# Kernel tuning notes

Hardware: AMD Instinct MI355X
Metric: run time of the kernel (lower is better)

Reference implementation:

```python
import jax, jax.numpy as jnp
import numpy as np

N_EMBD = 1024
HEADS = 16
HEAD_DIM = N_EMBD // HEADS


def setup_inputs() -> dict:
    key = jax.random.key(0)
    k1, k2 = jax.random.split(key)
    x = jax.random.normal(k1, (2, 2048, N_EMBD), dtype=jnp.float32)
    W_qkv = jax.random.normal(k2, (N_EMBD, 3 * N_EMBD), dtype=jnp.float32) * (N_EMBD ** -0.5)
    b_qkv = jnp.zeros((3 * N_EMBD,), dtype=jnp.float32)
    return {"x": x, "W_qkv": W_qkv, "b_qkv": b_qkv}


def reference(x, W_qkv, b_qkv):
    B, T, _ = x.shape
    qkv = x @ W_qkv + b_qkv                      # [B, T, 3*n_embd]
    q, k, v = jnp.split(qkv, 3, axis=-1)
    q = q.reshape(B, T, HEADS, HEAD_DIM)
    k = k.reshape(B, T, HEADS, HEAD_DIM)
    v = v.reshape(B, T, HEADS, HEAD_DIM)
    attn = jnp.einsum('bthd,bThd->bhtT', q, k) / jnp.sqrt(jnp.float32(HEAD_DIM))
    causal = jnp.tril(jnp.ones((T, T), dtype=bool))  # [T, T]
    attn = jnp.where(causal, attn, -jnp.inf)
    attn = jax.nn.softmax(attn, axis=-1)
    # dropout is identity in deterministic/eval mode (training=False)
    out = jnp.einsum('bhtT,bThd->bthd', attn, v).reshape(B, T, N_EMBD)
    return out
```

## Files before the change

### kernel.cpp

```cpp
#include <hip/hip_runtime.h>
#include <hip/hip_bf16.h>

#define BATCH 2
#define TSEQ  2048
#define NEMBD 1024
#define HEADS 16
#define HDIM  64

typedef short          bf16x8 __attribute__((ext_vector_type(8)));
typedef float          f32x4  __attribute__((ext_vector_type(4)));
typedef unsigned short u16;

__device__ __forceinline__ u16 f2bf(float f) {
  unsigned int u = __float_as_uint(f);
  u += 0x7fffu + ((u >> 16) & 1u);
  return (u16)(u >> 16);
}

__device__ __forceinline__ void gld16(const u16* g, u16* l) {
  __builtin_amdgcn_global_load_lds(
      (const __attribute__((address_space(1))) unsigned int*)g,
      (__attribute__((address_space(3))) unsigned int*)l, 16, 0, 0);
}

__global__ __launch_bounds__(256) void k_convert_x(const float* __restrict__ x,
                                                   u16* __restrict__ xb) {
  int i = blockIdx.x * 256 + threadIdx.x;
  float4 v = ((const float4*)x)[i];
  ushort4 o;
  o.x = f2bf(v.x); o.y = f2bf(v.y); o.z = f2bf(v.z); o.w = f2bf(v.w);
  ((ushort4*)xb)[i] = o;
}

__global__ __launch_bounds__(256) void k_transpose_w(const float* __restrict__ w,
                                                     u16* __restrict__ wt) {
  __shared__ float tile[32][33];
  const int n0 = blockIdx.x * 32;
  const int k0 = blockIdx.y * 32;
  const int t  = threadIdx.x;
  const int r  = t >> 3;
  const int c4 = (t & 7) * 4;
  float4 v = *(const float4*)(w + (size_t)(k0 + r) * 3072 + n0 + c4);
  tile[r][c4 + 0] = v.x; tile[r][c4 + 1] = v.y;
  tile[r][c4 + 2] = v.z; tile[r][c4 + 3] = v.w;
  __syncthreads();
  ushort4 o;
  o.x = f2bf(tile[c4 + 0][r]);
  o.y = f2bf(tile[c4 + 1][r]);
  o.z = f2bf(tile[c4 + 2][r]);
  o.w = f2bf(tile[c4 + 3][r]);
  *(ushort4*)(wt + (size_t)(n0 + r) * 1024 + k0 + c4) = o;
}

__global__ __launch_bounds__(256, 3) void k_qkv_gemm(
    const u16* __restrict__ xb, const u16* __restrict__ wt,
    const float* __restrict__ bias,
    u16* __restrict__ qb, u16* __restrict__ kbuf, u16* __restrict__ vt) {
  __shared__ __align__(16) u16 As[128 * 64];
  __shared__ __align__(16) u16 Bs[128 * 64];

  const int t    = threadIdx.x;
  const int wv   = t >> 6;
  const int lane = t & 63;
  const int m    = lane & 15;
  const int quad = lane >> 4;
  const int lin  = blockIdx.x;
  const int cp   = lin >> 5;
  const int rp   = ((lin & 7) << 2) | ((lin >> 3) & 3);
  const int row0 = rp * 128;
  const int col0 = cp * 128;
  const int wr   = (wv >> 1) * 64;
  const int wc   = (wv & 1) * 64;

  const int sr = wv * 32 + (lane >> 3);
  const int gs = (lane & 7) ^ (sr & 7);
  const u16* ag = xb + (size_t)(row0 + sr) * 1024 + gs * 8;
  const u16* bg = wt + (size_t)(col0 + sr) * 1024 + gs * 8;
  u16* al = As + (wv * 32) * 64;
  u16* bl = Bs + (wv * 32) * 64;

  f32x4 acc[4][4];
  const f32x4 zf = {0.f, 0.f, 0.f, 0.f};
  for (int i = 0; i < 4; ++i)
    for (int j = 0; j < 4; ++j) acc[i][j] = zf;

  for (int kt = 0; kt < 16; ++kt) {
    const int kk = kt * 64;
    __syncthreads();
    gld16(ag + kk,             al);
    gld16(ag + kk +  8 * 1024, al +  8 * 64);
    gld16(ag + kk + 16 * 1024, al + 16 * 64);
    gld16(ag + kk + 24 * 1024, al + 24 * 64);
    gld16(bg + kk,             bl);
    gld16(bg + kk +  8 * 1024, bl +  8 * 64);
    gld16(bg + kk + 16 * 1024, bl + 16 * 64);
    gld16(bg + kk + 24 * 1024, bl + 24 * 64);
    __syncthreads();

#pragma unroll
    for (int h = 0; h < 2; ++h) {
      const int g = ((quad + 4 * h) ^ (m & 7)) * 8;
      bf16x8 af[4], bfr[4];
#pragma unroll
      for (int mt = 0; mt < 4; ++mt)
        af[mt] = *(const bf16x8*)(As + (wr + mt * 16 + m) * 64 + g);
#pragma unroll
      for (int nt = 0; nt < 4; ++nt)
        bfr[nt] = *(const bf16x8*)(Bs + (wc + nt * 16 + m) * 64 + g);
#pragma unroll
      for (int mt = 0; mt < 4; ++mt)
#pragma unroll
        for (int nt = 0; nt < 4; ++nt)
          acc[mt][nt] = __builtin_amdgcn_mfma_f32_16x16x32_bf16(
              af[mt], bfr[nt], acc[mt][nt], 0, 0, 0);
    }
  }

  const int sec = col0 >> 10;
#pragma unroll
  for (int nt = 0; nt < 4; ++nt) {
    const int Cc = col0 + wc + nt * 16 + m;
    const float bv = bias[Cc];
    const int c = Cc & 1023;
    const int h = c >> 6;
    const int d = c & 63;
#pragma unroll
    for (int mt = 0; mt < 4; ++mt) {
      const int Rbase = row0 + wr + mt * 16 + quad * 4;
      const int bb = Rbase >> 11;
      const int t0 = Rbase & 2047;
      const int bh = bb * HEADS + h;
      if (sec == 0) {
#pragma unroll
        for (int rg = 0; rg < 4; ++rg) {
          float v = (acc[mt][nt][rg] + bv) * 0.125f;
          qb[(size_t)(bh * TSEQ + t0 + rg) * HDIM + d] = f2bf(v);
        }
      } else if (sec == 1) {
#pragma unroll
        for (int rg = 0; rg < 4; ++rg) {
          float v = acc[mt][nt][rg] + bv;
          kbuf[(size_t)(bh * TSEQ + t0 + rg) * HDIM + d] = f2bf(v);
        }
      } else {
        ushort4 pk;
        pk.x = f2bf(acc[mt][nt][0] + bv);
        pk.y = f2bf(acc[mt][nt][1] + bv);
        pk.z = f2bf(acc[mt][nt][2] + bv);
        pk.w = f2bf(acc[mt][nt][3] + bv);
        *(ushort4*)(vt + (size_t)(bh * HDIM + d) * TSEQ + t0) = pk;
      }
    }
  }
}

__global__ __launch_bounds__(256, 3) void k_attn(
    const u16* __restrict__ qb, const u16* __restrict__ kbuf,
    const u16* __restrict__ vt, float* __restrict__ out) {
  __shared__ __align__(16) u16 Kb[2][4096];
  __shared__ __align__(16) u16 Vb[2][4096];
  __shared__ __align__(16) u16 pt[4][2 * 1152];

  const int t     = threadIdx.x;
  const int wv    = t >> 6;
  const int lane  = t & 63;
  const int m     = lane & 15;
  const int quad  = lane >> 4;
  const int bh    = blockIdx.x & 31;
  const int qtg   = 15 - (blockIdx.x >> 5);
  const int qbase = (qtg * 4 + wv) * 32;
  const int nkt   = 2 * qtg + 2;
  const int maskTile = qbase >> 6;

  u16* pw0 = &pt[wv][0];
  u16* pw1 = &pt[wv][1152];

  const u16* qrow0 = qb + ((size_t)bh * TSEQ + qbase + m) * HDIM + quad * 8;
  const u16* qrow1 = qrow0 + 16 * HDIM;
  bf16x8 aq0g0 = *(const bf16x8*)(qrow0);
  bf16x8 aq1g0 = *(const bf16x8*)(qrow0 + 32);
  bf16x8 aq0g1 = *(const bf16x8*)(qrow1);
  bf16x8 aq1g1 = *(const bf16x8*)(qrow1 + 32);

  const int sr = wv * 16 + (lane >> 3);
  const int gs = (lane & 7) ^ (sr & 7);
  const u16* kg = kbuf + ((size_t)bh * TSEQ + sr) * HDIM + gs * 8;
  const u16* vg = vt + ((size_t)bh * HDIM + sr) * TSEQ + gs * 8;
  u16* klds = &Kb[0][wv * 16 * 64];
  u16* vlds = &Vb[0][wv * 16 * 64];

  const int swL = (quad ^ (m & 7)) * 8;
  const int swH = ((quad + 4) ^ (m & 7)) * 8;

  f32x4 o0[4], o1[4];
  const f32x4 zf = {0.f, 0.f, 0.f, 0.f};
  for (int nt = 0; nt < 4; ++nt) { o0[nt] = zf; o1[nt] = zf; }
  float rsum0 = 0.f, rsum1 = 0.f;
  const int qi0 = qbase + m;
  const int qi1 = qbase + 16 + m;

  gld16(kg,             klds);
  gld16(kg + 8 * HDIM,  klds + 8 * 64);
  gld16(vg,             vlds);
  gld16(vg + 8 * TSEQ,  vlds + 8 * 64);
  __syncthreads();

  for (int kt = 0; kt < nkt; ++kt) {
    const int b = kt & 1;
    const u16* kb0 = &Kb[b][0];
    const u16* vb0 = &Vb[b][0];
    const bool active = (kt <= maskTile);

    bf16x8 vfL[4], vfH[4];
    f32x4 s0[4], s1[4];

    if (active) {
      for (int nt = 0; nt < 4; ++nt) { s0[nt] = zf; s1[nt] = zf; }
#pragma unroll
      for (int nt = 0; nt < 4; ++nt) {
        bf16x8 kf = *(const bf16x8*)(kb0 + (nt * 16 + m) * 64 + swL);
        s0[nt] = __builtin_amdgcn_mfma_f32_16x16x32_bf16(kf, aq0g0, s0[nt], 0, 0, 0);
        s1[nt] = __builtin_amdgcn_mfma_f32_16x16x32_bf16(kf, aq0g1, s1[nt], 0, 0, 0);
      }
#pragma unroll
      for (int nt = 0; nt < 4; ++nt) {
        bf16x8 kf = *(const bf16x8*)(kb0 + (nt * 16 + m) * 64 + swH);
        s0[nt] = __builtin_amdgcn_mfma_f32_16x16x32_bf16(kf, aq1g0, s0[nt], 0, 0, 0);
        s1[nt] = __builtin_amdgcn_mfma_f32_16x16x32_bf16(kf, aq1g1, s1[nt], 0, 0, 0);
      }

      if (kt == maskTile) {
        const int kb_ = kt * 64 + quad * 4;
#pragma unroll
        for (int nt = 0; nt < 4; ++nt)
#pragma unroll
          for (int rg = 0; rg < 4; ++rg) {
            const int kj = kb_ + nt * 16 + rg;
            if (kj > qi0) s0[nt][rg] = -1e30f;
            if (kj > qi1) s1[nt][rg] = -1e30f;
          }
      }

#pragma unroll
      for (int nt = 0; nt < 4; ++nt) {
        float p0 = __expf(s0[nt][0]), p1 = __expf(s0[nt][1]);
        float p2 = __expf(s0[nt][2]), p3 = __expf(s0[nt][3]);
        rsum0 += (p0 + p1) + (p2 + p3);
        ushort4 pk = {f2bf(p0), f2bf(p1), f2bf(p2), f2bf(p3)};
        *(ushort4*)(pw0 + m * 72 + nt * 16 + quad * 4) = pk;
      }

#pragma unroll
      for (int nt = 0; nt < 4; ++nt) {
        vfL[nt] = *(const bf16x8*)(vb0 + (nt * 16 + m) * 64 + swL);
        vfH[nt] = *(const bf16x8*)(vb0 + (nt * 16 + m) * 64 + swH);
      }
    }

    if (kt + 1 < nkt) {
      const int nb = (kt + 1) & 1;
      const u16* kgn = kg + (size_t)(kt + 1) * 64 * HDIM;
      const u16* vgn = vg + (kt + 1) * 64;
      u16* kl = &Kb[nb][wv * 16 * 64];
      u16* vl = &Vb[nb][wv * 16 * 64];
      gld16(kgn,            kl);
      gld16(kgn + 8 * HDIM, kl + 8 * 64);
      gld16(vgn,            vl);
      gld16(vgn + 8 * TSEQ, vl + 8 * 64);
    }

    if (active) {
      bf16x8 bp00 = *(const bf16x8*)(pw0 + m * 72 + quad * 8);
      bf16x8 bp01 = *(const bf16x8*)(pw0 + m * 72 + 32 + quad * 8);
#pragma unroll
      for (int nt = 0; nt < 4; ++nt)
        o0[nt] = __builtin_amdgcn_mfma_f32_16x16x32_bf16(vfL[nt], bp00, o0[nt], 0, 0, 0);
#pragma unroll
      for (int nt = 0; nt < 4; ++nt)
        o0[nt] = __builtin_amdgcn_mfma_f32_16x16x32_bf16(vfH[nt], bp01, o0[nt], 0, 0, 0);

#pragma unroll
      for (int nt = 0; nt < 4; ++nt) {
        float p0 = __expf(s1[nt][0]), p1 = __expf(s1[nt][1]);
        float p2 = __expf(s1[nt][2]), p3 = __expf(s1[nt][3]);
        rsum1 += (p0 + p1) + (p2 + p3);
        ushort4 pk = {f2bf(p0), f2bf(p1), f2bf(p2), f2bf(p3)};
        *(ushort4*)(pw1 + m * 72 + nt * 16 + quad * 4) = pk;
      }
      bf16x8 bp10 = *(const bf16x8*)(pw1 + m * 72 + quad * 8);
      bf16x8 bp11 = *(const bf16x8*)(pw1 + m * 72 + 32 + quad * 8);
#pragma unroll
      for (int nt = 0; nt < 4; ++nt)
        o1[nt] = __builtin_amdgcn_mfma_f32_16x16x32_bf16(vfL[nt], bp10, o1[nt], 0, 0, 0);
#pragma unroll
      for (int nt = 0; nt < 4; ++nt)
        o1[nt] = __builtin_amdgcn_mfma_f32_16x16x32_bf16(vfH[nt], bp11, o1[nt], 0, 0, 0);
    }

    __syncthreads();
  }

  rsum0 += __shfl_xor(rsum0, 16);
  rsum0 += __shfl_xor(rsum0, 32);
  rsum1 += __shfl_xor(rsum1, 16);
  rsum1 += __shfl_xor(rsum1, 32);
  const float inv0 = 1.0f / rsum0;
  const float inv1 = 1.0f / rsum1;

  const int bb = bh >> 4;
  const int h  = bh & 15;
  float* ob0 = out + ((size_t)(bb * TSEQ + qi0) * NEMBD + h * HDIM + quad * 4);
  float* ob1 = out + ((size_t)(bb * TSEQ + qi1) * NEMBD + h * HDIM + quad * 4);
#pragma unroll
  for (int nt = 0; nt < 4; ++nt) {
    float4 st;
    st.x = o0[nt][0] * inv0; st.y = o0[nt][1] * inv0;
    st.z = o0[nt][2] * inv0; st.w = o0[nt][3] * inv0;
    *(float4*)(ob0 + nt * 16) = st;
    float4 su;
    su.x = o1[nt][0] * inv1; su.y = o1[nt][1] * inv1;
    su.z = o1[nt][2] * inv1; su.w = o1[nt][3] * inv1;
    *(float4*)(ob1 + nt * 16) = su;
  }
}

extern "C" void kernel_launch(void* const* d_in, const int* in_sizes, int n_in,
                              void* d_out, int out_size, void* d_ws, size_t ws_size,
                              hipStream_t stream) {
  (void)in_sizes; (void)n_in; (void)out_size; (void)ws_size;
  const float* x    = (const float*)d_in[0];
  const float* W    = (const float*)d_in[1];
  const float* bqkv = (const float*)d_in[2];
  float* out = (float*)d_out;

  u16* ws   = (u16*)d_ws;
  u16* qb   = ws;
  u16* kbuf = ws + 4194304;
  u16* vt   = ws + 2 * 4194304;
  u16* xb   = ws + 3 * 4194304;
  u16* wt   = ws + 4 * 4194304;

  hipLaunchKernelGGL(k_convert_x, dim3(4096), dim3(256), 0, stream, x, xb);
  hipLaunchKernelGGL(k_transpose_w, dim3(96, 32), dim3(256), 0, stream, W, wt);
  hipLaunchKernelGGL(k_qkv_gemm, dim3(768), dim3(256), 0, stream,
                     xb, wt, bqkv, qb, kbuf, vt);
  hipLaunchKernelGGL(k_attn, dim3(512), dim3(256), 0, stream,
                     qb, kbuf, vt, out);
}
```

Baseline: 149.7 us.

## Merge prep kernels and retile attention into 64-query blocks with balanced scheduling

```diff
diff --git a/kernel.cpp b/kernel.cpp
--- a/kernel.cpp
+++ b/kernel.cpp
@@ -23,33 +23,36 @@
       (__attribute__((address_space(3))) unsigned int*)l, 16, 0, 0);
 }
 
-__global__ __launch_bounds__(256) void k_convert_x(const float* __restrict__ x,
-                                                   u16* __restrict__ xb) {
-  int i = blockIdx.x * 256 + threadIdx.x;
-  float4 v = ((const float4*)x)[i];
-  ushort4 o;
-  o.x = f2bf(v.x); o.y = f2bf(v.y); o.z = f2bf(v.z); o.w = f2bf(v.w);
-  ((ushort4*)xb)[i] = o;
-}
-
-__global__ __launch_bounds__(256) void k_transpose_w(const float* __restrict__ w,
-                                                     u16* __restrict__ wt) {
+__global__ __launch_bounds__(256) void k_prep(const float* __restrict__ x,
+                                              u16* __restrict__ xb,
+                                              const float* __restrict__ w,
+                                              u16* __restrict__ wt) {
   __shared__ float tile[32][33];
-  const int n0 = blockIdx.x * 32;
-  const int k0 = blockIdx.y * 32;
-  const int t  = threadIdx.x;
-  const int r  = t >> 3;
-  const int c4 = (t & 7) * 4;
-  float4 v = *(const float4*)(w + (size_t)(k0 + r) * 3072 + n0 + c4);
-  tile[r][c4 + 0] = v.x; tile[r][c4 + 1] = v.y;
-  tile[r][c4 + 2] = v.z; tile[r][c4 + 3] = v.w;
-  __syncthreads();
-  ushort4 o;
-  o.x = f2bf(tile[c4 + 0][r]);
-  o.y = f2bf(tile[c4 + 1][r]);
-  o.z = f2bf(tile[c4 + 2][r]);
-  o.w = f2bf(tile[c4 + 3][r]);
-  *(ushort4*)(wt + (size_t)(n0 + r) * 1024 + k0 + c4) = o;
+  const int b = blockIdx.x;
+  const int t = threadIdx.x;
+  if (b < 4096) {
+    int i = b * 256 + t;
+    float4 v = ((const float4*)x)[i];
+    ushort4 o;
+    o.x = f2bf(v.x); o.y = f2bf(v.y); o.z = f2bf(v.z); o.w = f2bf(v.w);
+    ((ushort4*)xb)[i] = o;
+  } else {
+    const int bt = b - 4096;
+    const int n0 = (bt >> 5) * 32;
+    const int k0 = (bt & 31) * 32;
+    const int r  = t >> 3;
+    const int c4 = (t & 7) * 4;
+    float4 v = *(const float4*)(w + (size_t)(k0 + r) * 3072 + n0 + c4);
+    tile[r][c4 + 0] = v.x; tile[r][c4 + 1] = v.y;
+    tile[r][c4 + 2] = v.z; tile[r][c4 + 3] = v.w;
+    __syncthreads();
+    ushort4 o;
+    o.x = f2bf(tile[c4 + 0][r]);
+    o.y = f2bf(tile[c4 + 1][r]);
+    o.z = f2bf(tile[c4 + 2][r]);
+    o.w = f2bf(tile[c4 + 3][r]);
+    *(ushort4*)(wt + (size_t)(n0 + r) * 1024 + k0 + c4) = o;
+  }
 }
 
 __global__ __launch_bounds__(256, 3) void k_qkv_gemm(
@@ -154,12 +157,12 @@
   }
 }
 
-__global__ __launch_bounds__(256, 3) void k_attn(
+__global__ __launch_bounds__(128, 2) void k_attn(
     const u16* __restrict__ qb, const u16* __restrict__ kbuf,
     const u16* __restrict__ vt, float* __restrict__ out) {
   __shared__ __align__(16) u16 Kb[2][4096];
   __shared__ __align__(16) u16 Vb[2][4096];
-  __shared__ __align__(16) u16 pt[4][2 * 1152];
+  __shared__ __align__(16) u16 pt[2][2048];
 
   const int t     = threadIdx.x;
   const int wv    = t >> 6;
@@ -167,13 +170,19 @@
   const int m     = lane & 15;
   const int quad  = lane >> 4;
   const int bh    = blockIdx.x & 31;
-  const int qtg   = 15 - (blockIdx.x >> 5);
-  const int qbase = (qtg * 4 + wv) * 32;
-  const int nkt   = 2 * qtg + 2;
-  const int maskTile = qbase >> 6;
+  const int j     = blockIdx.x >> 5;
+  const int a_    = j & 7;
+  const int c_    = j >> 3;
+  int qg;
+  if      (c_ == 0) qg = 31 - a_;
+  else if (c_ == 1) qg = 16 + a_;
+  else if (c_ == 2) qg = 15 - a_;
+  else              qg = a_;
+  const int qbase = qg * 64 + wv * 32;
+  const int nkt   = qg + 1;
 
   u16* pw0 = &pt[wv][0];
-  u16* pw1 = &pt[wv][1152];
+  u16* pw1 = &pt[wv][1024];
 
   const u16* qrow0 = qb + ((size_t)bh * TSEQ + qbase + m) * HDIM + quad * 8;
   const u16* qrow1 = qrow0 + 16 * HDIM;
@@ -182,15 +191,21 @@
   bf16x8 aq0g1 = *(const bf16x8*)(qrow1);
   bf16x8 aq1g1 = *(const bf16x8*)(qrow1 + 32);
 
-  const int sr = wv * 16 + (lane >> 3);
+  const int sr = wv * 32 + (lane >> 3);
   const int gs = (lane & 7) ^ (sr & 7);
   const u16* kg = kbuf + ((size_t)bh * TSEQ + sr) * HDIM + gs * 8;
   const u16* vg = vt + ((size_t)bh * HDIM + sr) * TSEQ + gs * 8;
-  u16* klds = &Kb[0][wv * 16 * 64];
-  u16* vlds = &Vb[0][wv * 16 * 64];
+  u16* klds = &Kb[0][wv * 32 * 64];
+  u16* vlds = &Vb[0][wv * 32 * 64];
 
   const int swL = (quad ^ (m & 7)) * 8;
   const int swH = ((quad + 4) ^ (m & 7)) * 8;
+
+  const int pwr  = m * 64;
+  const int pwo  = (((0) * 2) * 8);
+  (void)pwo;
+  const int prdL = pwr + ((quad ^ (m & 7)) * 8);
+  const int prdH = pwr + (((quad + 4) ^ (m & 7)) * 8);
 
   f32x4 o0[4], o1[4];
   const f32x4 zf = {0.f, 0.f, 0.f, 0.f};
@@ -200,102 +215,106 @@
   const int qi1 = qbase + 16 + m;
 
   gld16(kg,             klds);
-  gld16(kg + 8 * HDIM,  klds + 8 * 64);
+  gld16(kg +  8 * HDIM, klds +  8 * 64);
+  gld16(kg + 16 * HDIM, klds + 16 * 64);
+  gld16(kg + 24 * HDIM, klds + 24 * 64);
   gld16(vg,             vlds);
-  gld16(vg + 8 * TSEQ,  vlds + 8 * 64);
+  gld16(vg +  8 * TSEQ, vlds +  8 * 64);
+  gld16(vg + 16 * TSEQ, vlds + 16 * 64);
+  gld16(vg + 24 * TSEQ, vlds + 24 * 64);
   __syncthreads();
 
   for (int kt = 0; kt < nkt; ++kt) {
     const int b = kt & 1;
     const u16* kb0 = &Kb[b][0];
     const u16* vb0 = &Vb[b][0];
-    const bool active = (kt <= maskTile);
+
+    f32x4 s0[4], s1[4];
+    for (int nt = 0; nt < 4; ++nt) { s0[nt] = zf; s1[nt] = zf; }
+#pragma unroll
+    for (int nt = 0; nt < 4; ++nt) {
+      bf16x8 kf = *(const bf16x8*)(kb0 + (nt * 16 + m) * 64 + swL);
+      s0[nt] = __builtin_amdgcn_mfma_f32_16x16x32_bf16(kf, aq0g0, s0[nt], 0, 0, 0);
+      s1[nt] = __builtin_amdgcn_mfma_f32_16x16x32_bf16(kf, aq0g1, s1[nt], 0, 0, 0);
+    }
+#pragma unroll
+    for (int nt = 0; nt < 4; ++nt) {
+      bf16x8 kf = *(const bf16x8*)(kb0 + (nt * 16 + m) * 64 + swH);
+      s0[nt] = __builtin_amdgcn_mfma_f32_16x16x32_bf16(kf, aq1g0, s0[nt], 0, 0, 0);
+      s1[nt] = __builtin_amdgcn_mfma_f32_16x16x32_bf16(kf, aq1g1, s1[nt], 0, 0, 0);
+    }
+
+    if (kt == nkt - 1) {
+      const int kb_ = kt * 64 + quad * 4;
+#pragma unroll
+      for (int nt = 0; nt < 4; ++nt)
+#pragma unroll
+        for (int rg = 0; rg < 4; ++rg) {
+          const int kj = kb_ + nt * 16 + rg;
+          if (kj > qi0) s0[nt][rg] = -1e30f;
+          if (kj > qi1) s1[nt][rg] = -1e30f;
+        }
+    }
+
+#pragma unroll
+    for (int nt = 0; nt < 4; ++nt) {
+      float p0 = __expf(s0[nt][0]), p1 = __expf(s0[nt][1]);
+      float p2 = __expf(s0[nt][2]), p3 = __expf(s0[nt][3]);
+      rsum0 += (p0 + p1) + (p2 + p3);
+      ushort4 pk = {f2bf(p0), f2bf(p1), f2bf(p2), f2bf(p3)};
+      *(ushort4*)(pw0 + pwr + (((nt * 2 + (quad >> 1)) ^ (m & 7)) * 8)
+                  + (quad & 1) * 4) = pk;
+    }
 
     bf16x8 vfL[4], vfH[4];
-    f32x4 s0[4], s1[4];
-
-    if (active) {
-      for (int nt = 0; nt < 4; ++nt) { s0[nt] = zf; s1[nt] = zf; }
-#pragma unroll
-      for (int nt = 0; nt < 4; ++nt) {
-        bf16x8 kf = *(const bf16x8*)(kb0 + (nt * 16 + m) * 64 + swL);
-        s0[nt] = __builtin_amdgcn_mfma_f32_16x16x32_bf16(kf, aq0g0, s0[nt], 0, 0, 0);
-        s1[nt] = __builtin_amdgcn_mfma_f32_16x16x32_bf16(kf, aq0g1, s1[nt], 0, 0, 0);
-      }
-#pragma unroll
-      for (int nt = 0; nt < 4; ++nt) {
-        bf16x8 kf = *(const bf16x8*)(kb0 + (nt * 16 + m) * 64 + swH);
-        s0[nt] = __builtin_amdgcn_mfma_f32_16x16x32_bf16(kf, aq1g0, s0[nt], 0, 0, 0);
-        s1[nt] = __builtin_amdgcn_mfma_f32_16x16x32_bf16(kf, aq1g1, s1[nt], 0, 0, 0);
-      }
-
-      if (kt == maskTile) {
-        const int kb_ = kt * 64 + quad * 4;
-#pragma unroll
-        for (int nt = 0; nt < 4; ++nt)
-#pragma unroll
-          for (int rg = 0; rg < 4; ++rg) {
-            const int kj = kb_ + nt * 16 + rg;
-            if (kj > qi0) s0[nt][rg] = -1e30f;
-            if (kj > qi1) s1[nt][rg] = -1e30f;
-          }
-      }
-
-#pragma unroll
-      for (int nt = 0; nt < 4; ++nt) {
-        float p0 = __expf(s0[nt][0]), p1 = __expf(s0[nt][1]);
-        float p2 = __expf(s0[nt][2]), p3 = __expf(s0[nt][3]);
-        rsum0 += (p0 + p1) + (p2 + p3);
-        ushort4 pk = {f2bf(p0), f2bf(p1), f2bf(p2), f2bf(p3)};
-        *(ushort4*)(pw0 + m * 72 + nt * 16 + quad * 4) = pk;
-      }
-
-#pragma unroll
-      for (int nt = 0; nt < 4; ++nt) {
-        vfL[nt] = *(const bf16x8*)(vb0 + (nt * 16 + m) * 64 + swL);
-        vfH[nt] = *(const bf16x8*)(vb0 + (nt * 16 + m) * 64 + swH);
-      }
+#pragma unroll
+    for (int nt = 0; nt < 4; ++nt) {
+      vfL[nt] = *(const bf16x8*)(vb0 + (nt * 16 + m) * 64 + swL);
+      vfH[nt] = *(const bf16x8*)(vb0 + (nt * 16 + m) * 64 + swH);
     }
 
     if (kt + 1 < nkt) {
       const int nb = (kt + 1) & 1;
       const u16* kgn = kg + (size_t)(kt + 1) * 64 * HDIM;
       const u16* vgn = vg + (kt + 1) * 64;
-      u16* kl = &Kb[nb][wv * 16 * 64];
-      u16* vl = &Vb[nb][wv * 16 * 64];
-      gld16(kgn,            kl);
-      gld16(kgn + 8 * HDIM, kl + 8 * 64);
-      gld16(vgn,            vl);
-      gld16(vgn + 8 * TSEQ, vl + 8 * 64);
-    }
-
-    if (active) {
-      bf16x8 bp00 = *(const bf16x8*)(pw0 + m * 72 + quad * 8);
-      bf16x8 bp01 = *(const bf16x8*)(pw0 + m * 72 + 32 + quad * 8);
-#pragma unroll
-      for (int nt = 0; nt < 4; ++nt)
-        o0[nt] = __builtin_amdgcn_mfma_f32_16x16x32_bf16(vfL[nt], bp00, o0[nt], 0, 0, 0);
-#pragma unroll
-      for (int nt = 0; nt < 4; ++nt)
-        o0[nt] = __builtin_amdgcn_mfma_f32_16x16x32_bf16(vfH[nt], bp01, o0[nt], 0, 0, 0);
-
-#pragma unroll
-      for (int nt = 0; nt < 4; ++nt) {
-        float p0 = __expf(s1[nt][0]), p1 = __expf(s1[nt][1]);
-        float p2 = __expf(s1[nt][2]), p3 = __expf(s1[nt][3]);
-        rsum1 += (p0 + p1) + (p2 + p3);
-        ushort4 pk = {f2bf(p0), f2bf(p1), f2bf(p2), f2bf(p3)};
-        *(ushort4*)(pw1 + m * 72 + nt * 16 + quad * 4) = pk;
-      }
-      bf16x8 bp10 = *(const bf16x8*)(pw1 + m * 72 + quad * 8);
-      bf16x8 bp11 = *(const bf16x8*)(pw1 + m * 72 + 32 + quad * 8);
-#pragma unroll
-      for (int nt = 0; nt < 4; ++nt)
-        o1[nt] = __builtin_amdgcn_mfma_f32_16x16x32_bf16(vfL[nt], bp10, o1[nt], 0, 0, 0);
-#pragma unroll
-      for (int nt = 0; nt < 4; ++nt)
-        o1[nt] = __builtin_amdgcn_mfma_f32_16x16x32_bf16(vfH[nt], bp11, o1[nt], 0, 0, 0);
-    }
+      u16* kl = &Kb[nb][wv * 32 * 64];
+      u16* vl = &Vb[nb][wv * 32 * 64];
+      gld16(kgn,             kl);
+      gld16(kgn +  8 * HDIM, kl +  8 * 64);
+      gld16(kgn + 16 * HDIM, kl + 16 * 64);
+      gld16(kgn + 24 * HDIM, kl + 24 * 64);
+      gld16(vgn,             vl);
+      gld16(vgn +  8 * TSEQ, vl +  8 * 64);
+      gld16(vgn + 16 * TSEQ, vl + 16 * 64);
+      gld16(vgn + 24 * TSEQ, vl + 24 * 64);
+    }
+
+    bf16x8 bp00 = *(const bf16x8*)(pw0 + prdL);
+    bf16x8 bp01 = *(const bf16x8*)(pw0 + prdH);
+#pragma unroll
+    for (int nt = 0; nt < 4; ++nt)
+      o0[nt] = __builtin_amdgcn_mfma_f32_16x16x32_bf16(vfL[nt], bp00, o0[nt], 0, 0, 0);
+#pragma unroll
+    for (int nt = 0; nt < 4; ++nt)
+      o0[nt] = __builtin_amdgcn_mfma_f32_16x16x32_bf16(vfH[nt], bp01, o0[nt], 0, 0, 0);
+
+#pragma unroll
+    for (int nt = 0; nt < 4; ++nt) {
+      float p0 = __expf(s1[nt][0]), p1 = __expf(s1[nt][1]);
+      float p2 = __expf(s1[nt][2]), p3 = __expf(s1[nt][3]);
+      rsum1 += (p0 + p1) + (p2 + p3);
+      ushort4 pk = {f2bf(p0), f2bf(p1), f2bf(p2), f2bf(p3)};
+      *(ushort4*)(pw1 + pwr + (((nt * 2 + (quad >> 1)) ^ (m & 7)) * 8)
+                  + (quad & 1) * 4) = pk;
+    }
+    bf16x8 bp10 = *(const bf16x8*)(pw1 + prdL);
+    bf16x8 bp11 = *(const bf16x8*)(pw1 + prdH);
+#pragma unroll
+    for (int nt = 0; nt < 4; ++nt)
+      o1[nt] = __builtin_amdgcn_mfma_f32_16x16x32_bf16(vfL[nt], bp10, o1[nt], 0, 0, 0);
+#pragma unroll
+    for (int nt = 0; nt < 4; ++nt)
+      o1[nt] = __builtin_amdgcn_mfma_f32_16x16x32_bf16(vfH[nt], bp11, o1[nt], 0, 0, 0);
 
     __syncthreads();
   }
@@ -340,10 +359,9 @@
   u16* xb   = ws + 3 * 4194304;
   u16* wt   = ws + 4 * 4194304;
 
-  hipLaunchKernelGGL(k_convert_x, dim3(4096), dim3(256), 0, stream, x, xb);
-  hipLaunchKernelGGL(k_transpose_w, dim3(96, 32), dim3(256), 0, stream, W, wt);
+  hipLaunchKernelGGL(k_prep, dim3(7168), dim3(256), 0, stream, x, xb, W, wt);
   hipLaunchKernelGGL(k_qkv_gemm, dim3(768), dim3(256), 0, stream,
                      xb, wt, bqkv, qb, kbuf, vt);
-  hipLaunchKernelGGL(k_attn, dim3(512), dim3(256), 0, stream,
+  hipLaunchKernelGGL(k_attn, dim3(1024), dim3(128), 0, stream,
                      qb, kbuf, vt, out);
 }
```

Result: no change. 147.3 us (-1.6%).
